# Kernel optimization log

Hardware: AMD Instinct MI355X
Metric: run time of the kernel (lower is better)

The kernel has to match this reference:

```python
import jax, jax.numpy as jnp
import numpy as np

B, T, I, H, O = 128, 512, 1024, 1024, 256


def setup_inputs() -> dict:
    key = jax.random.key(0)
    ks = jax.random.split(key, 8)
    return {
        "x": jax.random.normal(ks[0], (B, T, I), dtype=jnp.float32),
        "h0": jax.random.normal(ks[1], (B, H), dtype=jnp.float32),
        "c0": jax.random.normal(ks[2], (B, H), dtype=jnp.float32),
        "w_ih": jax.random.normal(ks[3], (4 * H, I), dtype=jnp.float32) * (1.0 / np.sqrt(I)),
        "w_hh": jax.random.normal(ks[4], (4 * H, H), dtype=jnp.float32) * (1.0 / np.sqrt(H)),
        "bias": jax.random.normal(ks[5], (4 * H,), dtype=jnp.float32) * 0.1,
        "w_fc": jax.random.normal(ks[6], (O, H), dtype=jnp.float32) * (1.0 / np.sqrt(H)),
        "b_fc": jax.random.normal(ks[7], (O,), dtype=jnp.float32) * 0.1,
    }


def reference(x, h0, c0, w_ih, w_hh, bias, w_fc, b_fc):
    # Precompute the input contribution to all gates with one big GEMM: [B,T,4H]
    x_gates = jnp.einsum('bti,gi->btg', x, w_ih) + bias

    def step(carry, xg_t):
        h, c = carry  # [B,H] each
        gates = xg_t + h @ w_hh.T  # [B,4H]
        i_g, f_g, g_g, o_g = jnp.split(gates, 4, axis=-1)
        i_g = jax.nn.sigmoid(i_g)
        f_g = jax.nn.sigmoid(f_g)
        g_g = jnp.tanh(g_g)
        o_g = jax.nn.sigmoid(o_g)
        c_next = f_g * c + i_g * g_g
        h_next = o_g * jnp.tanh(c_next)
        return (h_next, c_next), None

    (h_last, _), _ = jax.lax.scan(step, (h0, c0), jnp.swapaxes(x_gates, 0, 1))
    # Fused final FC on last hidden state
    return h_last @ w_fc.T + b_fc
```

## Files before the change

### kernel.cpp

```cpp
#include <hip/hip_runtime.h>
#include <hip/hip_bf16.h>


typedef float  v4f  __attribute__((ext_vector_type(4)));
typedef __bf16 v8bf __attribute__((ext_vector_type(8)));
typedef __bf16 v4bf __attribute__((ext_vector_type(4)));

#define NBLK_REC 128

static constexpr size_t XG_B    = (size_t)512 * 128 * 4096 * 2;
static constexpr size_t WIHP_O  = XG_B;
static constexpr size_t WHHP_O  = WIHP_O + (size_t)4096 * 1024 * 2;
static constexpr size_t BIASP_O = WHHP_O + (size_t)4096 * 1024 * 2;
static constexpr size_t HBUF_O  = BIASP_O + 16384;
static constexpr size_t XB_O    = HBUF_O + (size_t)2 * 128 * 512 * 8;
static constexpr size_t WS_FULL = XB_O + (size_t)128 * 512 * 1024 * 2;

__device__ __forceinline__ float bf2f(unsigned short u) {
    union { unsigned u32; float f; } c; c.u32 = (unsigned)u << 16; return c.f;
}

__global__ __launch_bounds__(256) void prep_kernel(
    const float* __restrict__ w_ih, const float* __restrict__ w_hh,
    const float* __restrict__ bias, const float* __restrict__ h0,
    __bf16* __restrict__ w_ihp, __bf16* __restrict__ w_hhp,
    float* __restrict__ biasp, unsigned long long* __restrict__ hb,
    int* __restrict__ unused)
{
    const int idx = blockIdx.x * 256 + threadIdx.x;
    const int n = idx >> 10, k = idx & 1023;
    const int hcol = (n >> 7) * 32 + ((n >> 5) & 3) * 8 + (n & 7);
    const int g = (n >> 3) & 3;
    const int on = g * 1024 + hcol;
    w_ihp[idx] = (__bf16)w_ih[(size_t)on * 1024 + k];
    w_hhp[idx] = (__bf16)w_hh[(size_t)on * 1024 + k];
    if (idx < 4096) {
        const int hc2 = (idx >> 7) * 32 + ((idx >> 5) & 3) * 8 + (idx & 7);
        biasp[idx] = bias[((idx >> 3) & 3) * 1024 + hc2];
    }
    if (idx < 128 * 512) {
        const int m = idx >> 9, jp = idx & 511;
        union { __bf16 b; unsigned short u; } c0h, c1h;
        c0h.b = (__bf16)h0[(size_t)m * 1024 + jp * 2];
        c1h.b = (__bf16)h0[(size_t)m * 1024 + jp * 2 + 1];
        hb[idx] = (unsigned long long)c0h.u | ((unsigned long long)c1h.u << 16);
        hb[65536 + idx] = 0xFFFFull << 32;
    }
    (void)unused;
}

__global__ __launch_bounds__(256) void xcast(
    const float* __restrict__ x, __bf16* __restrict__ xb)
{
    const size_t i = ((size_t)blockIdx.x * 256 + threadIdx.x) * 8;
    const float4 a = *(const float4*)&x[i];
    const float4 b = *(const float4*)&x[i + 4];
    v8bf o = { (__bf16)a.x, (__bf16)a.y, (__bf16)a.z, (__bf16)a.w,
               (__bf16)b.x, (__bf16)b.y, (__bf16)b.z, (__bf16)b.w };
    *(v8bf*)&xb[i] = o;
}

__global__ __launch_bounds__(256) void gemm_xg_bf16(
    const __bf16* __restrict__ xb, const __bf16* __restrict__ wih,
    const float* __restrict__ biasp, __bf16* __restrict__ xg)
{
    const int bx = blockIdx.x;
    const int mtile = bx >> 5, ntile = bx & 31;
    const int m0 = mtile << 7, n0 = ntile << 7;
    const int bb = mtile >> 2, t0 = (mtile & 3) << 7;
    const int tid = threadIdx.x;
    const int lane = tid & 63, wave = tid >> 6;
    const int wm = wave >> 1, wn = wave & 1;
    const int l15 = lane & 15, q = lane >> 4;

    __shared__ union {
        struct { __bf16 A[128][72]; __bf16 B[128][72]; } s;
        __bf16 C[128][132];
    } u;

    const int sr = tid >> 3, sc = (tid & 7) * 8;
    const __bf16* ag = xb  + (size_t)(m0 + sr) * 1024 + sc;
    const __bf16* bg = wih + (size_t)(n0 + sr) * 1024 + sc;

    v4f acc[4][4] = {};
    for (int kt = 0; kt < 16; ++kt) {
        __syncthreads();
        #pragma unroll
        for (int i = 0; i < 4; ++i) {
            *(v8bf*)&u.s.A[sr + i * 32][sc] = *(const v8bf*)(ag + (size_t)i * 32 * 1024 + kt * 64);
            *(v8bf*)&u.s.B[sr + i * 32][sc] = *(const v8bf*)(bg + (size_t)i * 32 * 1024 + kt * 64);
        }
        __syncthreads();
        v8bf a[2][4], b[2][4];
        #pragma unroll
        for (int ks = 0; ks < 2; ++ks) {
            #pragma unroll
            for (int im = 0; im < 4; ++im)
                a[ks][im] = *(const v8bf*)&u.s.A[wm * 64 + im * 16 + l15][ks * 32 + q * 8];
            #pragma unroll
            for (int in_ = 0; in_ < 4; ++in_)
                b[ks][in_] = *(const v8bf*)&u.s.B[wn * 64 + in_ * 16 + l15][ks * 32 + q * 8];
        }
        #pragma unroll
        for (int ks = 0; ks < 2; ++ks)
            #pragma unroll
            for (int im = 0; im < 4; ++im)
                #pragma unroll
                for (int in_ = 0; in_ < 4; ++in_)
                    acc[im][in_] = __builtin_amdgcn_mfma_f32_16x16x32_bf16(
                        a[ks][im], b[ks][in_], acc[im][in_], 0, 0, 0);
    }
    __syncthreads();
    #pragma unroll
    for (int in_ = 0; in_ < 4; ++in_) {
        const int nl = wn * 64 + in_ * 16 + l15;
        const int outl = (((nl >> 5) * 8 + (nl & 7)) << 2) | ((nl >> 3) & 3);
        const float bv = biasp[n0 + nl];
        #pragma unroll
        for (int im = 0; im < 4; ++im)
            #pragma unroll
            for (int r = 0; r < 4; ++r)
                u.C[wm * 64 + im * 16 + q * 4 + r][outl] = (__bf16)(acc[im][in_][r] + bv);
    }
    __syncthreads();
    const int cr = tid >> 1, chf = (tid & 1) * 64;
    __bf16* outp = xg + ((size_t)(t0 + cr) * 128 + bb) * 4096 + n0 + chf;
    #pragma unroll
    for (int j = 0; j < 8; ++j)
        *(uint4*)(outp + j * 8) = *(const uint4*)&u.C[cr][chf + j * 8];
}

__global__ __launch_bounds__(256) void gemm_xg_f32(
    const float* __restrict__ x, const __bf16* __restrict__ wih,
    const float* __restrict__ biasp, __bf16* __restrict__ xg)
{
    const int bx = blockIdx.x;
    const int mtile = bx >> 5, ntile = bx & 31;
    const int m0 = mtile << 7, n0 = ntile << 7;
    const int bb = mtile >> 2, t0 = (mtile & 3) << 7;
    const int tid = threadIdx.x;
    const int lane = tid & 63, wave = tid >> 6;
    const int wm = wave >> 1, wn = wave & 1;
    const int l15 = lane & 15, q = lane >> 4;

    __shared__ __bf16 Al[128][40];
    __shared__ __bf16 Bl[128][40];
    v4f acc[4][4] = {};

    for (int kt = 0; kt < 32; ++kt) {
        __syncthreads();
        const int k0 = kt * 32;
        #pragma unroll
        for (int i = 0; i < 4; ++i) {
            const int s = tid + i * 256, r = s >> 3, c = s & 7;
            const float4 v = *(const float4*)&x[(size_t)(m0 + r) * 1024 + k0 + c * 4];
            v4bf pk = { (__bf16)v.x, (__bf16)v.y, (__bf16)v.z, (__bf16)v.w };
            *(v4bf*)&Al[r][c * 4] = pk;
        }
        #pragma unroll
        for (int j = 0; j < 2; ++j) {
            const int s = tid + j * 256, r = s >> 2, ch = s & 3;
            const uint4 v = *(const uint4*)&wih[(size_t)(n0 + r) * 1024 + k0 + ch * 8];
            *(uint4*)&Bl[r][ch * 8] = v;
        }
        __syncthreads();
        v8bf a[4], b[4];
        #pragma unroll
        for (int im = 0; im < 4; ++im) a[im] = *(const v8bf*)&Al[wm * 64 + im * 16 + l15][q * 8];
        #pragma unroll
        for (int in_ = 0; in_ < 4; ++in_) b[in_] = *(const v8bf*)&Bl[wn * 64 + in_ * 16 + l15][q * 8];
        #pragma unroll
        for (int im = 0; im < 4; ++im)
            #pragma unroll
            for (int in_ = 0; in_ < 4; ++in_)
                acc[im][in_] = __builtin_amdgcn_mfma_f32_16x16x32_bf16(a[im], b[in_], acc[im][in_], 0, 0, 0);
    }
    #pragma unroll
    for (int in_ = 0; in_ < 4; ++in_) {
        const int nl = wn * 64 + in_ * 16 + l15;
        const int outl = (((nl >> 5) * 8 + (nl & 7)) << 2) | ((nl >> 3) & 3);
        const float bv = biasp[n0 + nl];
        #pragma unroll
        for (int im = 0; im < 4; ++im) {
            const int mbase = wm * 64 + im * 16 + q * 4;
            #pragma unroll
            for (int r = 0; r < 4; ++r)
                xg[((size_t)(t0 + mbase + r) * 128 + bb) * 4096 + n0 + outl] =
                    (__bf16)(acc[im][in_][r] + bv);
        }
    }
}

__device__ __forceinline__ float sigm_f(float x) {
    return __builtin_amdgcn_rcpf(1.f + __expf(-x));
}
__device__ __forceinline__ float tanh_f(float x) {
    return 1.f - 2.f * __builtin_amdgcn_rcpf(__expf(2.f * x) + 1.f);
}

__global__ __launch_bounds__(256, 1) void lstm_rec(
    const __bf16* __restrict__ whh, const __bf16* __restrict__ xg,
    const float* __restrict__ c0, unsigned long long* hbuf)
{
    const int tid  = threadIdx.x;
    const int lane = tid & 63, w = tid >> 6;
    const int l15  = lane & 15, q = lane >> 4;
    const int mq   = blockIdx.x >> 5;
    const int ns   = blockIdx.x & 31;

    __shared__ __bf16 hA[2][32][1032];

    v8bf breg[2][32];
    {
        const __bf16* wb = whh + (size_t)(ns * 128 + w * 32) * 1024;
        #pragma unroll
        for (int ni = 0; ni < 2; ++ni)
            #pragma unroll
            for (int kc = 0; kc < 32; ++kc)
                breg[ni][kc] = *(const v8bf*)&wb[(size_t)(ni * 16 + l15) * 1024 + kc * 32 + q * 8];
    }

    const int j    = l15 & 7;
    const int mi   = (l15 >> 3) & 1;
    const int hcol = ns * 32 + w * 8 + j;
    const int row0 = mi * 16 + q * 4;
    float c_[4];
    #pragma unroll
    for (int r = 0; r < 4; ++r)
        c_[r] = c0[(size_t)(mq * 32 + row0 + r) * 1024 + hcol];

    #pragma unroll 1
    for (int t = 1; t <= 512; ++t) {
        const int par  = (t - 1) & 1;
        const unsigned short want = (unsigned short)(t - 1);

        unsigned long long xq[4];
        {
            const unsigned long long* xp = (const unsigned long long*)xg
                + ((size_t)(t - 1) * 128 + mq * 32 + row0) * 1024 + hcol;
            #pragma unroll
            for (int r = 0; r < 4; ++r) xq[r] = xp[(size_t)r * 1024];
        }

        {
            const unsigned long long* hq = hbuf + (size_t)par * 65536;
            #pragma unroll 1
            for (int r2 = 0; r2 < 8; ++r2) {
                const int rowl = w * 8 + r2;
                const unsigned long long* base = hq + (size_t)(mq * 32 + rowl) * 512;
                unsigned long long gv[8];
                #pragma unroll
                for (int c = 0; c < 8; ++c)
                    gv[c] = __hip_atomic_load(base + c * 64 + lane,
                                              __ATOMIC_RELAXED, __HIP_MEMORY_SCOPE_AGENT);
                for (;;) {
                    bool ok = true;
                    #pragma unroll
                    for (int c = 0; c < 8; ++c)
                        ok &= ((unsigned short)(gv[c] >> 32) == want);
                    if (ok) break;
                    #pragma unroll
                    for (int c = 0; c < 8; ++c)
                        gv[c] = __hip_atomic_load(base + c * 64 + lane,
                                                  __ATOMIC_RELAXED, __HIP_MEMORY_SCOPE_AGENT);
                }
                #pragma unroll
                for (int c = 0; c < 8; ++c)
                    *(unsigned*)&hA[par][rowl][(c * 64 + lane) * 2] = (unsigned)gv[c];
            }
        }
        __syncthreads();

        v4f acc[2][2] = {};
        #pragma unroll
        for (int kc = 0; kc < 32; ++kc) {
            const v8bf a0 = *(const v8bf*)&hA[par][l15][kc * 32 + q * 8];
            const v8bf a1 = *(const v8bf*)&hA[par][l15 + 16][kc * 32 + q * 8];
            acc[0][0] = __builtin_amdgcn_mfma_f32_16x16x32_bf16(a0, breg[0][kc], acc[0][0], 0, 0, 0);
            acc[0][1] = __builtin_amdgcn_mfma_f32_16x16x32_bf16(a0, breg[1][kc], acc[0][1], 0, 0, 0);
            acc[1][0] = __builtin_amdgcn_mfma_f32_16x16x32_bf16(a1, breg[0][kc], acc[1][0], 0, 0, 0);
            acc[1][1] = __builtin_amdgcn_mfma_f32_16x16x32_bf16(a1, breg[1][kc], acc[1][1], 0, 0, 0);
        }

        v4f s0 = mi ? acc[0][0] : acc[1][0];
        v4f s1 = mi ? acc[0][1] : acc[1][1];
        v4f r0, r1;
        #pragma unroll
        for (int r = 0; r < 4; ++r) {
            r0[r] = __shfl_xor(s0[r], 8);
            r1[r] = __shfl_xor(s1[r], 8);
        }
        const v4f own0 = mi ? acc[1][0] : acc[0][0];
        const v4f own1 = mi ? acc[1][1] : acc[0][1];

        unsigned hw[4];
        #pragma unroll
        for (int r = 0; r < 4; ++r) {
            const float iv = (mi ? r0[r]   : own0[r]) + bf2f((unsigned short)(xq[r]));
            const float fv = (mi ? own0[r] : r0[r])   + bf2f((unsigned short)(xq[r] >> 16));
            const float gv = (mi ? r1[r]   : own1[r]) + bf2f((unsigned short)(xq[r] >> 32));
            const float ov = (mi ? own1[r] : r1[r])   + bf2f((unsigned short)(xq[r] >> 48));
            c_[r] = sigm_f(fv) * c_[r] + sigm_f(iv) * tanh_f(gv);
            const float hv = sigm_f(ov) * tanh_f(c_[r]);
            union { __bf16 b; unsigned short u; } cv; cv.b = (__bf16)hv;
            hw[r] = cv.u;
        }
        unsigned long long* hd = hbuf + (size_t)(t & 1) * 65536
                               + (size_t)(mq * 32 + row0) * 512 + (hcol >> 1);
        #pragma unroll
        for (int r = 0; r < 4; ++r) {
            const unsigned ph = __shfl_xor(hw[r], 1);
            if ((j & 1) == 0) {
                const unsigned long long wrd = (unsigned long long)(hw[r] | (ph << 16))
                                             | ((unsigned long long)(unsigned short)t << 32);
                __hip_atomic_store(hd + (size_t)r * 512, wrd,
                                   __ATOMIC_RELAXED, __HIP_MEMORY_SCOPE_AGENT);
            }
        }
    }
}

__global__ __launch_bounds__(256) void fc_out(
    const unsigned long long* __restrict__ hb, const float* __restrict__ wfc,
    const float* __restrict__ bfc, float* __restrict__ out)
{
    const int b = blockIdx.x, o = threadIdx.x;
    __shared__ float hs[1024];
    for (int i = threadIdx.x; i < 512; i += 256) {
        const unsigned long long g = hb[(size_t)b * 512 + i];
        hs[2 * i]     = bf2f((unsigned short)g);
        hs[2 * i + 1] = bf2f((unsigned short)(g >> 16));
    }
    __syncthreads();
    const float* wr = wfc + (size_t)o * 1024;
    float s = 0.f;
    for (int k = 0; k < 1024; k += 4) {
        const float4 w = *(const float4*)&wr[k];
        s += hs[k] * w.x + hs[k + 1] * w.y + hs[k + 2] * w.z + hs[k + 3] * w.w;
    }
    out[b * 256 + o] = s + bfc[o];
}

extern "C" void kernel_launch(void* const* d_in, const int* in_sizes, int n_in,
                              void* d_out, int out_size, void* d_ws, size_t ws_size,
                              hipStream_t stream) {
    (void)in_sizes; (void)n_in; (void)out_size;
    const float* x    = (const float*)d_in[0];
    const float* h0   = (const float*)d_in[1];
    const float* c0   = (const float*)d_in[2];
    const float* w_ih = (const float*)d_in[3];
    const float* w_hh = (const float*)d_in[4];
    const float* bias = (const float*)d_in[5];
    const float* w_fc = (const float*)d_in[6];
    const float* b_fc = (const float*)d_in[7];
    float* out = (float*)d_out;

    char* ws = (char*)d_ws;
    __bf16* xg    = (__bf16*)(ws);
    __bf16* w_ihp = (__bf16*)(ws + WIHP_O);
    __bf16* w_hhp = (__bf16*)(ws + WHHP_O);
    float*  biasp = (float*)(ws + BIASP_O);
    unsigned long long* hbuf = (unsigned long long*)(ws + HBUF_O);
    __bf16* xb    = (__bf16*)(ws + XB_O);

    prep_kernel<<<16384, 256, 0, stream>>>(w_ih, w_hh, bias, h0, w_ihp, w_hhp, biasp, hbuf, nullptr);
    if (ws_size >= WS_FULL) {
        xcast<<<32768, 256, 0, stream>>>(x, xb);
        gemm_xg_bf16<<<16384, 256, 0, stream>>>(xb, w_ihp, biasp, xg);
    } else {
        gemm_xg_f32<<<16384, 256, 0, stream>>>(x, w_ihp, biasp, xg);
    }
    lstm_rec<<<NBLK_REC, 256, 0, stream>>>(w_hhp, xg, c0, hbuf);
    fc_out<<<128, 256, 0, stream>>>(hbuf, w_fc, b_fc, out);
}
```

Baseline: 4.455 ms.

## Split LSTM recurrence across 256 blocks with narrower column slices

```diff
diff --git a/kernel.cpp b/kernel.cpp
--- a/kernel.cpp
+++ b/kernel.cpp
@@ -6,7 +6,7 @@
 typedef __bf16 v8bf __attribute__((ext_vector_type(8)));
 typedef __bf16 v4bf __attribute__((ext_vector_type(4)));
 
-#define NBLK_REC 128
+#define NBLK_REC 256
 
 static constexpr size_t XG_B    = (size_t)512 * 128 * 4096 * 2;
 static constexpr size_t WIHP_O  = XG_B;
@@ -24,19 +24,18 @@
     const float* __restrict__ w_ih, const float* __restrict__ w_hh,
     const float* __restrict__ bias, const float* __restrict__ h0,
     __bf16* __restrict__ w_ihp, __bf16* __restrict__ w_hhp,
-    float* __restrict__ biasp, unsigned long long* __restrict__ hb,
-    int* __restrict__ unused)
+    float* __restrict__ biasp, unsigned long long* __restrict__ hb)
 {
     const int idx = blockIdx.x * 256 + threadIdx.x;
     const int n = idx >> 10, k = idx & 1023;
-    const int hcol = (n >> 7) * 32 + ((n >> 5) & 3) * 8 + (n & 7);
-    const int g = (n >> 3) & 3;
+    const int hcol = (n >> 6) * 16 + ((n >> 4) & 3) * 4 + (n & 3);
+    const int g = (n >> 2) & 3;
     const int on = g * 1024 + hcol;
     w_ihp[idx] = (__bf16)w_ih[(size_t)on * 1024 + k];
     w_hhp[idx] = (__bf16)w_hh[(size_t)on * 1024 + k];
     if (idx < 4096) {
-        const int hc2 = (idx >> 7) * 32 + ((idx >> 5) & 3) * 8 + (idx & 7);
-        biasp[idx] = bias[((idx >> 3) & 3) * 1024 + hc2];
+        const int hc2 = (idx >> 6) * 16 + ((idx >> 4) & 3) * 4 + (idx & 3);
+        biasp[idx] = bias[((idx >> 2) & 3) * 1024 + hc2];
     }
     if (idx < 128 * 512) {
         const int m = idx >> 9, jp = idx & 511;
@@ -46,7 +45,6 @@
         hb[idx] = (unsigned long long)c0h.u | ((unsigned long long)c1h.u << 16);
         hb[65536 + idx] = 0xFFFFull << 32;
     }
-    (void)unused;
 }
 
 __global__ __launch_bounds__(256) void xcast(
@@ -114,7 +112,8 @@
     #pragma unroll
     for (int in_ = 0; in_ < 4; ++in_) {
         const int nl = wn * 64 + in_ * 16 + l15;
-        const int outl = (((nl >> 5) * 8 + (nl & 7)) << 2) | ((nl >> 3) & 3);
+        const int outl = ((nl >> 6) << 6) | ((((nl >> 4) & 3)) << 4)
+                       | ((nl & 3) << 2) | ((nl >> 2) & 3);
         const float bv = biasp[n0 + nl];
         #pragma unroll
         for (int im = 0; im < 4; ++im)
@@ -178,7 +177,8 @@
     #pragma unroll
     for (int in_ = 0; in_ < 4; ++in_) {
         const int nl = wn * 64 + in_ * 16 + l15;
-        const int outl = (((nl >> 5) * 8 + (nl & 7)) << 2) | ((nl >> 3) & 3);
+        const int outl = ((nl >> 6) << 6) | ((((nl >> 4) & 3)) << 4)
+                       | ((nl & 3) << 2) | ((nl >> 2) & 3);
         const float bv = biasp[n0 + nl];
         #pragma unroll
         for (int im = 0; im < 4; ++im) {
@@ -205,118 +205,98 @@
     const int tid  = threadIdx.x;
     const int lane = tid & 63, w = tid >> 6;
     const int l15  = lane & 15, q = lane >> 4;
-    const int mq   = blockIdx.x >> 5;
-    const int ns   = blockIdx.x & 31;
-
-    __shared__ __bf16 hA[2][32][1032];
-
-    v8bf breg[2][32];
+    const int mq   = blockIdx.x >> 6;
+    const int ns   = blockIdx.x & 63;
+
+    __shared__ __bf16 hA[32][1032];
+    __shared__ float  glds[4][32][21];
+
+    v8bf breg[32];
     {
-        const __bf16* wb = whh + (size_t)(ns * 128 + w * 32) * 1024;
-        #pragma unroll
-        for (int ni = 0; ni < 2; ++ni)
-            #pragma unroll
-            for (int kc = 0; kc < 32; ++kc)
-                breg[ni][kc] = *(const v8bf*)&wb[(size_t)(ni * 16 + l15) * 1024 + kc * 32 + q * 8];
-    }
-
-    const int j    = l15 & 7;
-    const int mi   = (l15 >> 3) & 1;
-    const int hcol = ns * 32 + w * 8 + j;
-    const int row0 = mi * 16 + q * 4;
-    float c_[4];
-    #pragma unroll
-    for (int r = 0; r < 4; ++r)
-        c_[r] = c0[(size_t)(mq * 32 + row0 + r) * 1024 + hcol];
+        const __bf16* wb = whh + (size_t)(ns * 64 + w * 16) * 1024;
+        #pragma unroll
+        for (int kc = 0; kc < 32; ++kc)
+            breg[kc] = *(const v8bf*)&wb[(size_t)l15 * 1024 + kc * 32 + q * 8];
+    }
+
+    const int em = lane & 31;
+    const int jp = lane >> 5;
+    const int hcolG = ns * 16 + w * 4 + jp * 2;
+    const int mG = mq * 32 + em;
+    float2 cv = *(const float2*)&c0[(size_t)mG * 1024 + hcolG];
 
     #pragma unroll 1
     for (int t = 1; t <= 512; ++t) {
         const int par  = (t - 1) & 1;
         const unsigned short want = (unsigned short)(t - 1);
 
-        unsigned long long xq[4];
-        {
-            const unsigned long long* xp = (const unsigned long long*)xg
-                + ((size_t)(t - 1) * 128 + mq * 32 + row0) * 1024 + hcol;
-            #pragma unroll
-            for (int r = 0; r < 4; ++r) xq[r] = xp[(size_t)r * 1024];
-        }
-
-        {
-            const unsigned long long* hq = hbuf + (size_t)par * 65536;
-            #pragma unroll 1
-            for (int r2 = 0; r2 < 8; ++r2) {
-                const int rowl = w * 8 + r2;
-                const unsigned long long* base = hq + (size_t)(mq * 32 + rowl) * 512;
-                unsigned long long gv[8];
+        const unsigned long long* xp = (const unsigned long long*)xg
+            + ((size_t)(t - 1) * 128 + mG) * 1024 + hcolG;
+        const unsigned long long xq0 = xp[0];
+        const unsigned long long xq1 = xp[1];
+
+        const unsigned long long* hq = hbuf + (size_t)par * 65536
+                                     + ((size_t)mq * 32 + w * 8) * 512;
+        unsigned long long gv[8][8];
+        #pragma unroll
+        for (int r = 0; r < 8; ++r)
+            #pragma unroll
+            for (int c = 0; c < 8; ++c)
+                gv[r][c] = __hip_atomic_load(hq + (size_t)r * 512 + c * 64 + lane,
+                                             __ATOMIC_RELAXED, __HIP_MEMORY_SCOPE_AGENT);
+        #pragma unroll
+        for (int r = 0; r < 8; ++r) {
+            for (;;) {
+                bool ok = true;
                 #pragma unroll
                 for (int c = 0; c < 8; ++c)
-                    gv[c] = __hip_atomic_load(base + c * 64 + lane,
-                                              __ATOMIC_RELAXED, __HIP_MEMORY_SCOPE_AGENT);
-                for (;;) {
-                    bool ok = true;
-                    #pragma unroll
-                    for (int c = 0; c < 8; ++c)
-                        ok &= ((unsigned short)(gv[c] >> 32) == want);
-                    if (ok) break;
-                    #pragma unroll
-                    for (int c = 0; c < 8; ++c)
-                        gv[c] = __hip_atomic_load(base + c * 64 + lane,
-                                                  __ATOMIC_RELAXED, __HIP_MEMORY_SCOPE_AGENT);
-                }
+                    ok &= ((unsigned short)(gv[r][c] >> 32) == want);
+                if (__builtin_expect(__ballot(ok) == ~0ull, 1)) break;
                 #pragma unroll
                 for (int c = 0; c < 8; ++c)
-                    *(unsigned*)&hA[par][rowl][(c * 64 + lane) * 2] = (unsigned)gv[c];
+                    gv[r][c] = __hip_atomic_load(hq + (size_t)r * 512 + c * 64 + lane,
+                                                 __ATOMIC_RELAXED, __HIP_MEMORY_SCOPE_AGENT);
             }
-        }
-        __syncthreads();
-
-        v4f acc[2][2] = {};
+            #pragma unroll
+            for (int c = 0; c < 8; ++c)
+                *(unsigned*)&hA[w * 8 + r][(c * 64 + lane) * 2] = (unsigned)gv[r][c];
+        }
+        __syncthreads();
+
+        v4f acc0 = {}, acc1 = {};
         #pragma unroll
         for (int kc = 0; kc < 32; ++kc) {
-            const v8bf a0 = *(const v8bf*)&hA[par][l15][kc * 32 + q * 8];
-            const v8bf a1 = *(const v8bf*)&hA[par][l15 + 16][kc * 32 + q * 8];
-            acc[0][0] = __builtin_amdgcn_mfma_f32_16x16x32_bf16(a0, breg[0][kc], acc[0][0], 0, 0, 0);
-            acc[0][1] = __builtin_amdgcn_mfma_f32_16x16x32_bf16(a0, breg[1][kc], acc[0][1], 0, 0, 0);
-            acc[1][0] = __builtin_amdgcn_mfma_f32_16x16x32_bf16(a1, breg[0][kc], acc[1][0], 0, 0, 0);
-            acc[1][1] = __builtin_amdgcn_mfma_f32_16x16x32_bf16(a1, breg[1][kc], acc[1][1], 0, 0, 0);
-        }
-
-        v4f s0 = mi ? acc[0][0] : acc[1][0];
-        v4f s1 = mi ? acc[0][1] : acc[1][1];
-        v4f r0, r1;
+            const v8bf a0 = *(const v8bf*)&hA[l15][kc * 32 + q * 8];
+            const v8bf a1 = *(const v8bf*)&hA[l15 + 16][kc * 32 + q * 8];
+            acc0 = __builtin_amdgcn_mfma_f32_16x16x32_bf16(a0, breg[kc], acc0, 0, 0, 0);
+            acc1 = __builtin_amdgcn_mfma_f32_16x16x32_bf16(a1, breg[kc], acc1, 0, 0, 0);
+        }
+
         #pragma unroll
         for (int r = 0; r < 4; ++r) {
-            r0[r] = __shfl_xor(s0[r], 8);
-            r1[r] = __shfl_xor(s1[r], 8);
-        }
-        const v4f own0 = mi ? acc[1][0] : acc[0][0];
-        const v4f own1 = mi ? acc[1][1] : acc[0][1];
-
-        unsigned hw[4];
-        #pragma unroll
-        for (int r = 0; r < 4; ++r) {
-            const float iv = (mi ? r0[r]   : own0[r]) + bf2f((unsigned short)(xq[r]));
-            const float fv = (mi ? own0[r] : r0[r])   + bf2f((unsigned short)(xq[r] >> 16));
-            const float gv = (mi ? r1[r]   : own1[r]) + bf2f((unsigned short)(xq[r] >> 32));
-            const float ov = (mi ? own1[r] : r1[r])   + bf2f((unsigned short)(xq[r] >> 48));
-            c_[r] = sigm_f(fv) * c_[r] + sigm_f(iv) * tanh_f(gv);
-            const float hv = sigm_f(ov) * tanh_f(c_[r]);
-            union { __bf16 b; unsigned short u; } cv; cv.b = (__bf16)hv;
-            hw[r] = cv.u;
-        }
-        unsigned long long* hd = hbuf + (size_t)(t & 1) * 65536
-                               + (size_t)(mq * 32 + row0) * 512 + (hcol >> 1);
-        #pragma unroll
-        for (int r = 0; r < 4; ++r) {
-            const unsigned ph = __shfl_xor(hw[r], 1);
-            if ((j & 1) == 0) {
-                const unsigned long long wrd = (unsigned long long)(hw[r] | (ph << 16))
-                                             | ((unsigned long long)(unsigned short)t << 32);
-                __hip_atomic_store(hd + (size_t)r * 512, wrd,
-                                   __ATOMIC_RELAXED, __HIP_MEMORY_SCOPE_AGENT);
-            }
-        }
+            glds[w][q * 4 + r][l15]      = acc0[r];
+            glds[w][16 + q * 4 + r][l15] = acc1[r];
+        }
+        float g0[4], g1[4];
+        #pragma unroll
+        for (int g = 0; g < 4; ++g) {
+            g0[g] = glds[w][em][g * 4 + jp * 2]
+                  + bf2f((unsigned short)(xq0 >> (16 * g)));
+            g1[g] = glds[w][em][g * 4 + jp * 2 + 1]
+                  + bf2f((unsigned short)(xq1 >> (16 * g)));
+        }
+        cv.x = sigm_f(g0[1]) * cv.x + sigm_f(g0[0]) * tanh_f(g0[2]);
+        cv.y = sigm_f(g1[1]) * cv.y + sigm_f(g1[0]) * tanh_f(g1[2]);
+        const float hx = sigm_f(g0[3]) * tanh_f(cv.x);
+        const float hy = sigm_f(g1[3]) * tanh_f(cv.y);
+
+        union { __bf16 b[2]; unsigned u; } hp;
+        hp.b[0] = (__bf16)hx; hp.b[1] = (__bf16)hy;
+        const unsigned long long wrd = (unsigned long long)hp.u
+                                     | ((unsigned long long)(unsigned short)t << 32);
+        __hip_atomic_store(
+            hbuf + (size_t)(t & 1) * 65536 + (size_t)mG * 512 + (hcolG >> 1),
+            wrd, __ATOMIC_RELAXED, __HIP_MEMORY_SCOPE_AGENT);
     }
 }
 
@@ -363,7 +343,7 @@
     unsigned long long* hbuf = (unsigned long long*)(ws + HBUF_O);
     __bf16* xb    = (__bf16*)(ws + XB_O);
 
-    prep_kernel<<<16384, 256, 0, stream>>>(w_ih, w_hh, bias, h0, w_ihp, w_hhp, biasp, hbuf, nullptr);
+    prep_kernel<<<16384, 256, 0, stream>>>(w_ih, w_hh, bias, h0, w_ihp, w_hhp, biasp, hbuf);
     if (ws_size >= WS_FULL) {
         xcast<<<32768, 256, 0, stream>>>(x, xb);
         gemm_xg_bf16<<<16384, 256, 0, stream>>>(xb, w_ihp, biasp, xg);
```

Result: slower. 5.991 ms (+34.5%).
